# Kernel optimization log

Measured on AMD Instinct MI355X. Metric: run time of the kernel, lower is better.

Reference implementation:

```python
import jax, jax.numpy as jnp
import numpy as np

B, S, T = 2, 4096, 4096
SRC, DST, WIDTH = 512, 512, 128
BLK = 128  # JAKAL_ADDITIVE_ROUTE_BLOCK_SIZE default


def setup_inputs() -> dict:
    key = jax.random.key(0)
    ks = jax.random.split(key, 7)
    return {
        "source_val": jax.random.normal(ks[0], (B, S, SRC), jnp.float32),
        "target_val": jax.random.normal(ks[1], (B, T, DST), jnp.float32),
        "Ws": jax.random.normal(ks[2], (WIDTH, SRC), jnp.float32) * 0.02,  # source_proj weight
        "Wt": jax.random.normal(ks[3], (WIDTH, DST), jnp.float32) * 0.02,  # target_proj weight
        "ws_out": jax.random.normal(ks[4], (WIDTH,), jnp.float32) * 0.02,  # source_out weight
        "wt_out": jax.random.normal(ks[5], (WIDTH,), jnp.float32) * 0.02,  # target_out weight
        "w_int": jax.random.normal(ks[6], (WIDTH,), jnp.float32) * 0.02,   # interaction_weight
        "bias": jnp.zeros((), jnp.float32),
    }


def reference(source_val, target_val, Ws, Wt, ws_out, wt_out, w_int, bias):
    # Projections (Linear without bias): y = x @ W.T
    ps = jnp.einsum('bsd,wd->bsw', source_val, Ws)   # [B,S,WIDTH]
    pt = jnp.einsum('btd,wd->btw', target_val, Wt)   # [B,T,WIDTH]
    s_lin = jnp.einsum('bsw,w->bs', ps, ws_out)      # [B,S]
    t_lin = jnp.einsum('btw,w->bt', pt, wt_out)      # [B,T]

    nblk = S // BLK
    # Block the source axis, matching the torch block loop (avoids a [B,S,T,W] tensor).
    ps_blocks = ps.reshape(B, nblk, BLK, WIDTH).transpose(1, 0, 2, 3)   # [nblk,B,BLK,W]
    sl_blocks = s_lin.reshape(B, nblk, BLK).transpose(1, 0, 2)          # [nblk,B,BLK]

    def block_scores(_, xs):
        ps_blk, sl_blk = xs
        # SiLU of the elementwise bilinear interaction, then low-rank weighted reduce.
        inter = jax.nn.silu(ps_blk[:, :, None, :] * pt[:, None, :, :])  # [B,BLK,T,W]
        sc = jnp.einsum('bktw,w->bkt', inter, w_int)
        sc = sc + sl_blk[:, :, None] + t_lin[:, None, :] + bias
        return None, sc

    _, out = jax.lax.scan(block_scores, None, (ps_blocks, sl_blocks))   # [nblk,B,BLK,T]
    return out.transpose(1, 0, 2, 3).reshape(B, S, T)
```

## Files before the change

### kernel.cpp

```cpp
#include <hip/hip_runtime.h>
#include <cstdint>
#include <cstddef>

#define B_ 2
#define S_ 4096
#define T_ 4096
#define D_ 512
#define W_ 128

#define A0C (-0.0006958f)
#define A1C (0.2529946f)
#define A2C (-0.0226345f)
#define A3C (0.0022173f)
#define A4C (-0.00011668f)
#define ZCUT 2.5f
#define ROWCAP 65536

typedef __attribute__((ext_vector_type(8))) short bf16x8;
typedef __attribute__((ext_vector_type(4))) float f32x4;

__device__ __forceinline__ uint16_t f2bf(float f){
  uint32_t u = __float_as_uint(f);
  u += 0x7FFFu + ((u >> 16) & 1u);
  return (uint16_t)(u >> 16);
}
__device__ __forceinline__ float bf2f(uint16_t h){
  return __uint_as_float(((uint32_t)h) << 16);
}

__device__ __forceinline__ void gl_lds16(const void* g, void* l){
  __builtin_amdgcn_global_load_lds(
      (const __attribute__((address_space(1))) void*)g,
      (__attribute__((address_space(3))) void*)l, 16, 0, 0);
}

union F4 { float4 v; float f[4]; };

template<int INBF>
__global__ void prep_k(const void* __restrict__ Ws, const void* __restrict__ Wt,
                       const void* __restrict__ wso, const void* __restrict__ wto,
                       const void* __restrict__ wi, const void* __restrict__ bias,
                       float* __restrict__ WsT, float* __restrict__ WtT,
                       float* __restrict__ wsof, float* __restrict__ wtof,
                       float* __restrict__ wif, float* __restrict__ cbias,
                       int* __restrict__ rowCnt){
  auto cv = [](const void* p, int i)->float{
    if (INBF) return bf2f(((const uint16_t*)p)[i]);
    return ((const float*)p)[i];
  };
  const void* in = (blockIdx.x & 1) ? Wt : Ws;
  float* out = (blockIdx.x & 1) ? WtT : WsT;
  int base = (blockIdx.x >> 1) * 4096;
  for (int o = base + threadIdx.x; o < base + 4096; o += blockDim.x){
    int d = o >> 7, w = o & (W_ - 1);
    out[o] = cv(in, w * D_ + d);
  }
  if (blockIdx.x == 0){
    if (threadIdx.x < W_){
      wsof[threadIdx.x] = cv(wso, threadIdx.x);
      wtof[threadIdx.x] = cv(wto, threadIdx.x);
      wif[threadIdx.x]  = cv(wi,  threadIdx.x);
    }
    __syncthreads();
    if (threadIdx.x == 0){
      float s = 0.f;
      for (int k = 0; k < W_; ++k) s += wif[k];
      cbias[0] = cv(bias, 0) + A0C * s;
      rowCnt[0] = 0;
    }
  }
}

template<int INBF, int MODE>
__global__ __launch_bounds__(256) void proj_k(const void* __restrict__ xraw,
        const float* __restrict__ WT, const float* __restrict__ wout,
        const float* __restrict__ wint,
        float* __restrict__ pT, float* __restrict__ lin,
        uint16_t* __restrict__ feat){
  __shared__ float xl[64 * 36];
  __shared__ float wl[64 * 128];
  int tid = threadIdx.x;
  int tx = tid & 31, ty = tid >> 5;
  int rowBase = blockIdx.x * 32;
  float acc[4][4] = {};
  for (int c = 0; c < 8; ++c){
    int d0 = c * 64;
    const float4* wt4 = (const float4*)(WT + (size_t)d0 * W_);
    float4* wl4 = (float4*)wl;
    #pragma unroll
    for (int p = 0; p < 8; ++p){ int q = tid + 256 * p; wl4[q] = wt4[q]; }
    #pragma unroll
    for (int p = 0; p < 2; ++p){
      int q = tid + 256 * p;
      int r = q >> 4, dq = q & 15;
      float v0, v1, v2, v3;
      if (INBF){
        const uint16_t* xp = (const uint16_t*)xraw + (size_t)(rowBase + r) * D_ + d0 + dq * 4;
        ushort4 u = *(const ushort4*)xp;
        v0 = bf2f(u.x); v1 = bf2f(u.y); v2 = bf2f(u.z); v3 = bf2f(u.w);
      } else {
        const float* xp = (const float*)xraw + (size_t)(rowBase + r) * D_ + d0 + dq * 4;
        float4 u = *(const float4*)xp;
        v0 = u.x; v1 = u.y; v2 = u.z; v3 = u.w;
      }
      xl[(dq*4+0)*36 + r] = v0;
      xl[(dq*4+1)*36 + r] = v1;
      xl[(dq*4+2)*36 + r] = v2;
      xl[(dq*4+3)*36 + r] = v3;
    }
    __syncthreads();
    #pragma unroll 4
    for (int d = 0; d < 64; ++d){
      F4 a, w;
      a.v = *(const float4*)(xl + d * 36 + ty * 4);
      w.v = *(const float4*)(wl + d * 128 + tx * 4);
      #pragma unroll
      for (int i = 0; i < 4; ++i)
        #pragma unroll
        for (int j = 0; j < 4; ++j)
          acc[i][j] = fmaf(a.f[i], w.f[j], acc[i][j]);
    }
    __syncthreads();
  }
  float* tile = wl;
  #pragma unroll
  for (int i = 0; i < 4; ++i)
    #pragma unroll
    for (int j = 0; j < 4; ++j)
      tile[(tx*4 + j) * 33 + ty*4 + i] = acc[i][j];
  F4 wo; wo.v = *(const float4*)(wout + tx * 4);
  F4 wiv;
  if (MODE == 0) wiv.v = *(const float4*)(wint + tx * 4);
  #pragma unroll
  for (int i = 0; i < 4; ++i){
    int r = rowBase + ty * 4 + i;
    float s = acc[i][0]*wo.f[0] + acc[i][1]*wo.f[1] + acc[i][2]*wo.f[2] + acc[i][3]*wo.f[3];
    #pragma unroll
    for (int off = 16; off >= 1; off >>= 1) s += __shfl_xor(s, off, 32);
    if (tx == 0) lin[r] = s;
    ushort4 g[5];
    uint16_t* gp = (uint16_t*)g;
    #pragma unroll
    for (int j = 0; j < 4; ++j){
      float p = acc[i][j];
      float p2 = p*p, p4 = p2*p2, p6 = p4*p2, p8 = p4*p4;
      float e0, e1, e2, e3, e4;
      if (MODE == 0){
        float wq = wiv.f[j];
        e0 = 0.5f * wq * p; e1 = A1C * wq * p2; e2 = A2C * wq * p4;
        e3 = A3C * wq * p6; e4 = A4C * wq * p8;
      } else {
        e0 = p; e1 = p2; e2 = p4; e3 = p6; e4 = p8;
      }
      gp[0*4+j] = f2bf(e0); gp[1*4+j] = f2bf(e1); gp[2*4+j] = f2bf(e2);
      gp[3*4+j] = f2bf(e3); gp[4*4+j] = f2bf(e4);
    }
    uint16_t* o = feat + (size_t)r * 640 + tx * 4;
    *(ushort4*)(o)       = g[0];
    *(ushort4*)(o + 128) = g[1];
    *(ushort4*)(o + 256) = g[2];
    *(ushort4*)(o + 384) = g[3];
    *(ushort4*)(o + 512) = g[4];
  }
  __syncthreads();
  {
    int w = tid >> 1, h = tid & 1;
    int b = rowBase >> 12;
    int sb = rowBase & (S_ - 1);
    float* dst = pT + ((size_t)(b * W_ + w)) * S_ + sb + h * 16;
    const float* src = tile + w * 33 + h * 16;
    #pragma unroll
    for (int k = 0; k < 4; ++k){
      float4 o = make_float4(src[k*4+0], src[k*4+1], src[k*4+2], src[k*4+3]);
      *(float4*)(dst + k * 4) = o;
    }
  }
}

__global__ void maxT_k(const float* __restrict__ ptT, float* __restrict__ maxT){
  int bw = blockIdx.x;
  int tid = threadIdx.x;
  const float* c = ptT + (size_t)bw * T_;
  float m = 0.f;
  for (int t = tid; t < T_; t += 256) m = fmaxf(m, fabsf(c[t]));
  #pragma unroll
  for (int off = 32; off >= 1; off >>= 1) m = fmaxf(m, __shfl_xor(m, off, 64));
  __shared__ float red[4];
  if ((tid & 63) == 0) red[tid >> 6] = m;
  __syncthreads();
  if (tid == 0)
    maxT[bw] = fmaxf(fmaxf(red[0], red[1]), fmaxf(red[2], red[3]));
}

template<int OUTBF>
__global__ __launch_bounds__(256) void gemm_k(const uint16_t* __restrict__ fA,
      const uint16_t* __restrict__ fB, const float* __restrict__ slin,
      const float* __restrict__ tlin, const float* __restrict__ cbias,
      void* __restrict__ outv){
  __shared__ __align__(16) uint16_t As[128 * 32];
  __shared__ __align__(16) uint16_t Bs[128 * 32];
  int tid = threadIdx.x, lane = tid & 63, wv = tid >> 6;
  int quad = lane >> 4, lr = lane & 15;
  int rowT = blockIdx.y * 128, colT = blockIdx.x * 128;
  int b = rowT >> 12;
  int r0 = lane >> 2, c0 = (lane & 3) * 8;
  int mBase = (wv & 1) * 64, nBase = (wv >> 1) * 64;

  f32x4 acc[4][4];
  #pragma unroll
  for (int i = 0; i < 4; ++i)
    #pragma unroll
    for (int j = 0; j < 4; ++j)
      acc[i][j] = (f32x4){0.f, 0.f, 0.f, 0.f};

  const uint16_t* aBase = fA + (size_t)rowT * 640;
  const uint16_t* bBase = fB + ((size_t)b * T_ + colT) * 640;

  for (int step = 0; step < 20; ++step){
    int kc = step * 32;
    #pragma unroll
    for (int h = 0; h < 2; ++h){
      int q = 2 * wv + h;
      gl_lds16(aBase + (size_t)(16 * q + r0) * 640 + kc + c0, &As[q * 512]);
      gl_lds16(bBase + (size_t)(16 * q + r0) * 640 + kc + c0, &Bs[q * 512]);
    }
    __syncthreads();
    bf16x8 af[4], bfr[4];
    #pragma unroll
    for (int i = 0; i < 4; ++i)
      af[i] = *(const bf16x8*)&As[(mBase + i * 16 + lr) * 32 + quad * 8];
    #pragma unroll
    for (int j = 0; j < 4; ++j)
      bfr[j] = *(const bf16x8*)&Bs[(nBase + j * 16 + lr) * 32 + quad * 8];
    #pragma unroll
    for (int i = 0; i < 4; ++i)
      #pragma unroll
      for (int j = 0; j < 4; ++j)
        acc[i][j] = __builtin_amdgcn_mfma_f32_16x16x32_bf16(bfr[j], af[i], acc[i][j], 0, 0, 0);
    __syncthreads();
  }

  float cb = cbias[0];
  #pragma unroll
  for (int i = 0; i < 4; ++i){
    int srow = rowT + mBase + i * 16 + lr;
    float sl = slin[srow] + cb;
    #pragma unroll
    for (int j = 0; j < 4; ++j){
      int t0 = colT + nBase + j * 16 + quad * 4;
      F4 tl; tl.v = *(const float4*)(tlin + b * T_ + t0);
      float o0 = acc[i][j][0] + sl + tl.f[0];
      float o1 = acc[i][j][1] + sl + tl.f[1];
      float o2 = acc[i][j][2] + sl + tl.f[2];
      float o3 = acc[i][j][3] + sl + tl.f[3];
      size_t oi = (size_t)srow * T_ + t0;
      if (OUTBF){
        ushort4 pk = make_ushort4(f2bf(o0), f2bf(o1), f2bf(o2), f2bf(o3));
        *(ushort4*)((uint16_t*)outv + oi) = pk;
      } else {
        *(float4*)((float*)outv + oi) = make_float4(o0, o1, o2, o3);
      }
    }
  }
}

__global__ void flagrows_k(const float* __restrict__ psT, const float* __restrict__ maxT,
                           uint32_t* __restrict__ rowList, int* __restrict__ rowCnt){
  int w = blockIdx.x, b = blockIdx.y;
  int tid = threadIdx.x;
  float mt = maxT[b * W_ + w];
  const float* psc = psT + (size_t)(b * W_ + w) * S_;
  for (int s = tid; s < S_; s += 256){
    float p = psc[s];
    if (fabsf(p) * mt > ZCUT){
      int k = atomicAdd(rowCnt, 1);
      if (k < ROWCAP)
        rowList[k] = ((uint32_t)b << 19) | ((uint32_t)w << 12) | (uint32_t)s;
    }
  }
}

template<int OUTBF>
__global__ __launch_bounds__(256) void fixscan_k(const float* __restrict__ psT,
        const float* __restrict__ ptT, const float* __restrict__ wint,
        const uint16_t* __restrict__ fA, const uint16_t* __restrict__ fB,
        const uint32_t* __restrict__ rowList, const int* __restrict__ rowCnt,
        void* __restrict__ outv){
  int n = *rowCnt; if (n > ROWCAP) n = ROWCAP;
  int tid = threadIdx.x;
  for (int job = blockIdx.x; job < n; job += gridDim.x){
    uint32_t pk = rowList[job];
    int b = (int)(pk >> 19), w = (int)((pk >> 12) & 127u), s = (int)(pk & 4095u);
    float wi = wint[w];
    float p = psT[(size_t)(b * W_ + w) * S_ + s];
    const float* ptc = ptT + (size_t)(b * W_ + w) * T_;
    const uint16_t* fa = fA + ((size_t)b * S_ + s) * 640 + w;
    float a0 = bf2f(fa[0]),   a1 = bf2f(fa[128]), a2 = bf2f(fa[256]);
    float a3 = bf2f(fa[384]), a4 = bf2f(fa[512]);
    for (int t = tid; t < T_; t += 256){
      float q = ptc[t];
      float z = p * q;
      if (fabsf(z) > ZCUT){
        const uint16_t* fb = fB + ((size_t)b * T_ + t) * 640 + w;
        float dot = a0 * bf2f(fb[0]) + a1 * bf2f(fb[128]) + a2 * bf2f(fb[256])
                  + a3 * bf2f(fb[384]) + a4 * bf2f(fb[512]);
        float sil = z / (1.0f + __expf(-z));
        float corr = wi * sil - dot - A0C * wi;
        size_t idx = ((size_t)b * S_ + s) * T_ + t;
        if (OUTBF){
          uint32_t* wp = (uint32_t*)outv + (idx >> 1);
          bool hi = (idx & 1u) != 0;
          uint32_t assumed, old = *wp;
          do {
            assumed = old;
            uint16_t h = hi ? (uint16_t)(assumed >> 16) : (uint16_t)(assumed & 0xFFFFu);
            uint16_t nh = f2bf(bf2f(h) + corr);
            uint32_t nw = hi ? ((assumed & 0x0000FFFFu) | ((uint32_t)nh << 16))
                             : ((assumed & 0xFFFF0000u) | (uint32_t)nh);
            old = atomicCAS(wp, assumed, nw);
          } while (old != assumed);
        } else {
          atomicAdd((float*)outv + idx, corr);
        }
      }
    }
  }
}

extern "C" void kernel_launch(void* const* d_in, const int* in_sizes, int n_in,
                              void* d_out, int out_size, void* d_ws, size_t ws_size,
                              hipStream_t stream){
  char* ws = (char*)d_ws;
  size_t off = 0;
  auto alloc = [&](size_t bytes)->char*{
    char* p = ws + off; off += (bytes + 255) & ~(size_t)255; return p;
  };
  float*    WsT  = (float*)   alloc((size_t)D_*W_*4);
  float*    WtT  = (float*)   alloc((size_t)D_*W_*4);
  float*    wsof = (float*)   alloc(W_*4);
  float*    wtof = (float*)   alloc(W_*4);
  float*    wif  = (float*)   alloc(W_*4);
  float*    cbias= (float*)   alloc(4);
  int*      rowCnt=(int*)     alloc(4);
  uint32_t* rowList=(uint32_t*)alloc((size_t)ROWCAP*4);
  float*    psT  = (float*)   alloc((size_t)B_*S_*W_*4);
  float*    ptT  = (float*)   alloc((size_t)B_*T_*W_*4);
  float*    slin = (float*)   alloc((size_t)B_*S_*4);
  float*    tlin = (float*)   alloc((size_t)B_*T_*4);
  float*    maxT = (float*)   alloc((size_t)B_*W_*4);
  uint16_t* featA= (uint16_t*)alloc((size_t)B_*S_*640*2);
  uint16_t* featB= (uint16_t*)alloc((size_t)B_*T_*640*2);

  bool inbf  = (in_sizes[0] == (int)((size_t)B_*S_*D_*2));
  bool outbf = (out_size    == (int)((size_t)B_*S_*T_*2));

  if (inbf){
    hipLaunchKernelGGL((prep_k<1>), dim3(32), dim3(256), 0, stream,
        d_in[2], d_in[3], d_in[4], d_in[5], d_in[6], d_in[7],
        WsT, WtT, wsof, wtof, wif, cbias, rowCnt);
    hipLaunchKernelGGL((proj_k<1,0>), dim3(B_*S_/32), dim3(256), 0, stream,
        d_in[0], WsT, wsof, wif, psT, slin, featA);
    hipLaunchKernelGGL((proj_k<1,1>), dim3(B_*T_/32), dim3(256), 0, stream,
        d_in[1], WtT, wtof, wif, ptT, tlin, featB);
  } else {
    hipLaunchKernelGGL((prep_k<0>), dim3(32), dim3(256), 0, stream,
        d_in[2], d_in[3], d_in[4], d_in[5], d_in[6], d_in[7],
        WsT, WtT, wsof, wtof, wif, cbias, rowCnt);
    hipLaunchKernelGGL((proj_k<0,0>), dim3(B_*S_/32), dim3(256), 0, stream,
        d_in[0], WsT, wsof, wif, psT, slin, featA);
    hipLaunchKernelGGL((proj_k<0,1>), dim3(B_*T_/32), dim3(256), 0, stream,
        d_in[1], WtT, wtof, wif, ptT, tlin, featB);
  }
  hipLaunchKernelGGL(maxT_k, dim3(B_*W_), dim3(256), 0, stream, ptT, maxT);
  if (outbf)
    hipLaunchKernelGGL((gemm_k<1>), dim3(T_/128, B_*S_/128), dim3(256), 0, stream,
        featA, featB, slin, tlin, cbias, d_out);
  else
    hipLaunchKernelGGL((gemm_k<0>), dim3(T_/128, B_*S_/128), dim3(256), 0, stream,
        featA, featB, slin, tlin, cbias, d_out);
  hipLaunchKernelGGL(flagrows_k, dim3(W_, B_), dim3(256), 0, stream,
      psT, maxT, rowList, rowCnt);
  if (outbf)
    hipLaunchKernelGGL((fixscan_k<1>), dim3(2048), dim3(256), 0, stream,
        psT, ptT, wif, featA, featB, rowList, rowCnt, d_out);
  else
    hipLaunchKernelGGL((fixscan_k<0>), dim3(2048), dim3(256), 0, stream,
        psT, ptT, wif, featA, featB, rowList, rowCnt, d_out);
}
```

Before: 325.5 us.

## Double-buffer LDS tiles in bf16 GEMM to overlap global loads with MFMA

```diff
diff --git a/kernel.cpp b/kernel.cpp
--- a/kernel.cpp
+++ b/kernel.cpp
@@ -197,8 +197,8 @@
       const uint16_t* __restrict__ fB, const float* __restrict__ slin,
       const float* __restrict__ tlin, const float* __restrict__ cbias,
       void* __restrict__ outv){
-  __shared__ __align__(16) uint16_t As[128 * 32];
-  __shared__ __align__(16) uint16_t Bs[128 * 32];
+  __shared__ __align__(16) uint16_t As[2][128 * 32];
+  __shared__ __align__(16) uint16_t Bs[2][128 * 32];
   int tid = threadIdx.x, lane = tid & 63, wv = tid >> 6;
   int quad = lane >> 4, lr = lane & 15;
   int rowT = blockIdx.y * 128, colT = blockIdx.x * 128;
@@ -216,28 +216,41 @@
   const uint16_t* aBase = fA + (size_t)rowT * 640;
   const uint16_t* bBase = fB + ((size_t)b * T_ + colT) * 640;
 
-  for (int step = 0; step < 20; ++step){
-    int kc = step * 32;
-    #pragma unroll
-    for (int h = 0; h < 2; ++h){
-      int q = 2 * wv + h;
-      gl_lds16(aBase + (size_t)(16 * q + r0) * 640 + kc + c0, &As[q * 512]);
-      gl_lds16(bBase + (size_t)(16 * q + r0) * 640 + kc + c0, &Bs[q * 512]);
-    }
-    __syncthreads();
+  const int NSTEP = 20;
+  #pragma unroll
+  for (int h = 0; h < 2; ++h){
+    int q = 2 * wv + h;
+    gl_lds16(aBase + (size_t)(16 * q + r0) * 640 + c0, &As[0][q * 512]);
+    gl_lds16(bBase + (size_t)(16 * q + r0) * 640 + c0, &Bs[0][q * 512]);
+  }
+  for (int step = 0; step < NSTEP; ++step){
+    int cur = step & 1;
+    if (step + 1 < NSTEP){
+      int kc = (step + 1) * 32;
+      #pragma unroll
+      for (int h = 0; h < 2; ++h){
+        int q = 2 * wv + h;
+        gl_lds16(aBase + (size_t)(16 * q + r0) * 640 + kc + c0, &As[cur ^ 1][q * 512]);
+        gl_lds16(bBase + (size_t)(16 * q + r0) * 640 + kc + c0, &Bs[cur ^ 1][q * 512]);
+      }
+      asm volatile("s_waitcnt vmcnt(4)" ::: "memory");
+    } else {
+      asm volatile("s_waitcnt vmcnt(0)" ::: "memory");
+    }
+    __builtin_amdgcn_s_barrier();
     bf16x8 af[4], bfr[4];
     #pragma unroll
     for (int i = 0; i < 4; ++i)
-      af[i] = *(const bf16x8*)&As[(mBase + i * 16 + lr) * 32 + quad * 8];
+      af[i] = *(const bf16x8*)&As[cur][(mBase + i * 16 + lr) * 32 + quad * 8];
     #pragma unroll
     for (int j = 0; j < 4; ++j)
-      bfr[j] = *(const bf16x8*)&Bs[(nBase + j * 16 + lr) * 32 + quad * 8];
+      bfr[j] = *(const bf16x8*)&Bs[cur][(nBase + j * 16 + lr) * 32 + quad * 8];
     #pragma unroll
     for (int i = 0; i < 4; ++i)
       #pragma unroll
       for (int j = 0; j < 4; ++j)
         acc[i][j] = __builtin_amdgcn_mfma_f32_16x16x32_bf16(bfr[j], af[i], acc[i][j], 0, 0, 0);
-    __syncthreads();
+    __builtin_amdgcn_s_barrier();
   }
 
   float cb = cbias[0];
```

Result: faster. 314.9 us (-3.3%).
